# Kernel optimization log

Hardware: AMD Instinct MI355X
Metric: run time of the kernel (lower is better)

Reference implementation:

```python
import jax, jax.numpy as jnp
import numpy as np

B = 8192        # batch
F = 16          # num_fields
V = 50000       # vocab per field
D = 32          # embed_dim (all equal per assert)
NE = 3          # number of embedding spaces
NL = 3          # cross-net layers
EOD = F * D     # 512 = embed_output_dim
M1, M2, M3 = 512, 256, 128
REG_WEIGHT = 0.01


def setup_inputs() -> dict:
    key = jax.random.key(0)
    ks = jax.random.split(key, 12)
    x = jax.random.randint(ks[0], (B, F), 0, V)
    emb_tables = jax.random.normal(ks[1], (NE, F * V, D), dtype=jnp.float32) * 0.05
    cross_W = jax.random.normal(ks[2], (NE, NL, EOD, EOD), dtype=jnp.float32) * (1.0 / np.sqrt(EOD))
    cross_b = jnp.zeros((NE, NL, EOD), dtype=jnp.float32)
    mlp1_W = jax.random.normal(ks[3], (NE, EOD, M1), dtype=jnp.float32) * (1.0 / np.sqrt(EOD))
    mlp1_b = jnp.zeros((NE, M1), dtype=jnp.float32)
    mlp_W1 = jax.random.normal(ks[4], (M1, M2), dtype=jnp.float32) * (1.0 / np.sqrt(M1))
    mlp_b1 = jnp.zeros((M2,), dtype=jnp.float32)
    mlp_W2 = jax.random.normal(ks[5], (M2, M3), dtype=jnp.float32) * (1.0 / np.sqrt(M2))
    mlp_b2 = jnp.zeros((M3,), dtype=jnp.float32)
    mlp_W3 = jax.random.normal(ks[6], (M3, 1), dtype=jnp.float32) * (1.0 / np.sqrt(M3))
    mlp_b3 = jnp.zeros((1,), dtype=jnp.float32)
    return {"x": x, "emb_tables": emb_tables, "cross_W": cross_W, "cross_b": cross_b,
            "mlp1_W": mlp1_W, "mlp1_b": mlp1_b, "mlp_W1": mlp_W1, "mlp_b1": mlp_b1,
            "mlp_W2": mlp_W2, "mlp_b2": mlp_b2, "mlp_W3": mlp_W3, "mlp_b3": mlp_b3}


def _branch(x0, Ws, bs, W1, b1):
    # DCNv2 cross network: x_{l+1} = x0 * (W_l x_l + b_l) + x_l, then one MLP layer (ReLU)
    xl = x0
    for l in range(NL):
        xl = x0 * (xl @ Ws[l] + bs[l]) + xl
    return jax.nn.relu(xl @ W1 + b1)


def reference(x, emb_tables, cross_W, cross_b, mlp1_W, mlp1_b,
              mlp_W1, mlp_b1, mlp_W2, mlp_b2, mlp_W3, mlp_b3):
    offsets = jnp.arange(F, dtype=x.dtype) * V
    idx = x + offsets                      # [B, F] indices into shared table
    es = emb_tables[:, idx]                # [NE, B, F, D]
    es_flat = es.reshape(NE, B, EOD)       # [NE, B, F*D]
    h = jax.vmap(_branch)(es_flat, cross_W, cross_b, mlp1_W, mlp1_b)  # [NE, B, M1]
    h = h.mean(axis=0)                     # mean over embedding spaces
    h = jax.nn.relu(h @ mlp_W1 + mlp_b1)
    h = jax.nn.relu(h @ mlp_W2 + mlp_b2)
    p = h @ mlp_W3 + mlp_b3                # [B, 1]
    output = jax.nn.sigmoid(p[:, 0])
    # training-path regularizer: per-field cross-embedding Gram SVDs
    pairs = [(1, 0), (2, 0), (2, 1)]
    sims = []
    for i, j in pairs:
        m = jnp.einsum('bkd,bke->kde', es[i], es[j])     # [F, D, D]
        s = jnp.linalg.svd(m, compute_uv=False)          # batched singular values [F, D]
        sims.append(s.mean(axis=0))                      # [D]
    sim = jnp.concatenate(sims)                          # [len(pairs)*D]
    reg_loss = REG_WEIGHT * jnp.mean(sim ** 2)
    return output, reg_loss
```

## Files before the change

kernel.cpp:

```cpp
#include <hip/hip_runtime.h>
#include <math.h>

#define B_ 8192
#define F_ 16
#define V_ 50000
#define D_ 32
#define NE_ 3
#define EOD_ 512
#define M1_ 512
#define M2_ 256
#define M3_ 128
#define BE_ ((size_t)B_ * EOD_)

typedef __attribute__((ext_vector_type(8))) short short8;
typedef __attribute__((ext_vector_type(4))) float floatx4;

__device__ __forceinline__ unsigned short f2bf(float f) {
    union { float f; unsigned u; } v; v.f = f;
    unsigned r = v.u + 0x7FFF + ((v.u >> 16) & 1);
    return (unsigned short)(r >> 16);
}
__device__ __forceinline__ float bf2f(unsigned short h) {
    union { unsigned u; float f; } v; v.u = (unsigned)h << 16;
    return v.f;
}
__device__ __forceinline__ void gld16(const void* g, void* l) {
    __builtin_amdgcn_global_load_lds(
        (const __attribute__((address_space(1))) unsigned int*)g,
        (__attribute__((address_space(3))) unsigned int*)l, 16, 0, 0);
}

__global__ __launch_bounds__(256) void gather_k(const int* __restrict__ x,
    const float* __restrict__ tables, unsigned short* __restrict__ esb)
{
    int gid = blockIdx.x * 256 + threadIdx.x;
    int d8 = gid & 3;
    int f  = (gid >> 2) & 15;
    int b  = (gid >> 6) & (B_ - 1);
    int e  = gid >> 19;
    int idx = x[b * F_ + f] + f * V_;
    const float4* src = (const float4*)(tables + ((size_t)e * F_ * V_ + idx) * D_) + d8 * 2;
    float4 v0 = src[0], v1 = src[1];
    unsigned short o[8];
    o[0] = f2bf(v0.x); o[1] = f2bf(v0.y); o[2] = f2bf(v0.z); o[3] = f2bf(v0.w);
    o[4] = f2bf(v1.x); o[5] = f2bf(v1.y); o[6] = f2bf(v1.z); o[7] = f2bf(v1.w);
    unsigned short* dst = esb + ((size_t)e * B_ + b) * EOD_ + f * D_ + d8 * 8;
    *(uint4*)dst = *(uint4*)o;
}

__global__ __launch_bounds__(256) void wtrans12_k(const float* __restrict__ crossW,
    const float* __restrict__ mlp1W, unsigned short* __restrict__ Wt)
{
    __shared__ float tile[32][33];
    int bn = blockIdx.x * 32, bk = blockIdx.y * 32;
    int mat = blockIdx.z;
    const float* Wm = (mat < 9) ? crossW + (size_t)mat * 512 * 512
                                : mlp1W + (size_t)(mat - 9) * 512 * 512;
    unsigned short* Wtm = Wt + (size_t)mat * 512 * 512;
    int tx = threadIdx.x & 31, ty = threadIdx.x >> 5;
    #pragma unroll
    for (int i = 0; i < 32; i += 8)
        tile[ty + i][tx] = Wm[(size_t)(bk + ty + i) * 512 + bn + tx];
    __syncthreads();
    #pragma unroll
    for (int i = 0; i < 32; i += 8)
        Wtm[(size_t)(bn + ty + i) * 512 + bk + tx] = f2bf(tile[tx][ty + i]);
}

__global__ __launch_bounds__(256) void wtrans_k(const float* __restrict__ W,
    unsigned short* __restrict__ Wt, int K, int N)
{
    __shared__ float tile[32][33];
    int bn = blockIdx.x * 32, bk = blockIdx.y * 32;
    int tx = threadIdx.x & 31, ty = threadIdx.x >> 5;
    #pragma unroll
    for (int i = 0; i < 32; i += 8)
        tile[ty + i][tx] = W[(size_t)(bk + ty + i) * N + bn + tx];
    __syncthreads();
    #pragma unroll
    for (int i = 0; i < 32; i += 8)
        Wt[(size_t)(bn + ty + i) * K + bk + tx] = f2bf(tile[tx][ty + i]);
}

__global__ __launch_bounds__(256) void gemm_mfma_k(
    const unsigned short* __restrict__ A,  long sA,
    const unsigned short* __restrict__ Wt, long sW,
    const float* __restrict__ bias,        long sB,
    const unsigned short* __restrict__ x0, long sX,
    const unsigned short* __restrict__ xl, long sXl,
    unsigned short* __restrict__ outb,     long sO,
    int M, int N, int K, int mode)
{
    int e = blockIdx.z;
    A    += (size_t)e * sA;
    Wt   += (size_t)e * sW;
    bias += (size_t)e * sB;
    outb += (size_t)e * sO;
    if (mode == 0) { x0 += (size_t)e * sX; xl += (size_t)e * sXl; }

    __shared__ unsigned short As[128 * 32];
    __shared__ unsigned short Bs[128 * 32];
    int t = threadIdx.x;
    int w = t >> 6, lane = t & 63;
    int quad = lane >> 4, lid = lane & 15;
    int wr = (w & 1) * 64, wc = (w >> 1) * 64;
    int rowbase = blockIdx.y * 128, colbase = blockIdx.x * 128;

    int chunk = w * 2;
    int sub = lane >> 2;
    int kk = (lane & 3) * 8;
    const unsigned short* pa0 = A  + (size_t)(rowbase + chunk * 16 + sub) * K + kk;
    const unsigned short* pa1 = pa0 + (size_t)16 * K;
    const unsigned short* pb0 = Wt + (size_t)(colbase + chunk * 16 + sub) * K + kk;
    const unsigned short* pb1 = pb0 + (size_t)16 * K;
    unsigned short* la0 = As + chunk * 512 + lane * 8;
    unsigned short* la1 = la0 + 512;
    unsigned short* lb0 = Bs + chunk * 512 + lane * 8;
    unsigned short* lb1 = lb0 + 512;

    floatx4 acc[4][4];
    #pragma unroll
    for (int i = 0; i < 4; i++)
        #pragma unroll
        for (int j = 0; j < 4; j++) acc[i][j] = {0.f, 0.f, 0.f, 0.f};

    for (int k0 = 0; k0 < K; k0 += 32) {
        if (k0) __syncthreads();
        gld16(pa0 + k0, la0);
        gld16(pa1 + k0, la1);
        gld16(pb0 + k0, lb0);
        gld16(pb1 + k0, lb1);
        __syncthreads();
        short8 af[4], bfr[4];
        #pragma unroll
        for (int i = 0; i < 4; i++) {
            af[i]  = *(const short8*)(As + (wr + i * 16 + lid) * 32 + quad * 8);
            bfr[i] = *(const short8*)(Bs + (wc + i * 16 + lid) * 32 + quad * 8);
        }
        #pragma unroll
        for (int i = 0; i < 4; i++)
            #pragma unroll
            for (int j = 0; j < 4; j++)
                acc[i][j] = __builtin_amdgcn_mfma_f32_16x16x32_bf16(af[i], bfr[j], acc[i][j], 0, 0, 0);
    }

    #pragma unroll
    for (int i = 0; i < 4; i++) {
        int row0 = rowbase + wr + i * 16 + quad * 4;
        #pragma unroll
        for (int j = 0; j < 4; j++) {
            int col = colbase + wc + j * 16 + lid;
            float bv = bias[col];
            #pragma unroll
            for (int rr = 0; rr < 4; rr++) {
                size_t off = (size_t)(row0 + rr) * N + col;
                float v = acc[i][j][rr] + bv;
                if (mode == 0)      v = bf2f(x0[off]) * v + bf2f(xl[off]);
                else if (mode == 1) v = fmaxf(v, 0.f) * (1.f / 3.f);
                else                v = fmaxf(v, 0.f);
                outb[off] = f2bf(v);
            }
        }
    }
}

__global__ __launch_bounds__(256) void sum3_k(const unsigned short* __restrict__ h,
                                              unsigned short* __restrict__ o)
{
    size_t i = ((size_t)blockIdx.x * 256 + threadIdx.x) * 8;
    uint4 a = *(const uint4*)(h + i);
    uint4 b = *(const uint4*)(h + BE_ + i);
    uint4 c = *(const uint4*)(h + 2 * BE_ + i);
    const unsigned short* pa = (const unsigned short*)&a;
    const unsigned short* pb = (const unsigned short*)&b;
    const unsigned short* pc = (const unsigned short*)&c;
    unsigned short r[8];
    #pragma unroll
    for (int j = 0; j < 8; j++) r[j] = f2bf(bf2f(pa[j]) + bf2f(pb[j]) + bf2f(pc[j]));
    *(uint4*)(o + i) = *(uint4*)r;
}

__global__ __launch_bounds__(256) void final_k(const unsigned short* __restrict__ h2,
    const float* __restrict__ W3, const float* __restrict__ b3,
    float* __restrict__ out)
{
    int gt = blockIdx.x * 256 + threadIdx.x;
    int s = gt >> 6, lane = gt & 63;
    float p = bf2f(h2[(size_t)s * 128 + lane]) * W3[lane]
            + bf2f(h2[(size_t)s * 128 + 64 + lane]) * W3[64 + lane];
    #pragma unroll
    for (int off = 32; off > 0; off >>= 1) p += __shfl_down(p, off);
    if (lane == 0) out[s] = 1.0f / (1.0f + expf(-(p + b3[0])));
}

__global__ __launch_bounds__(256) void pairsum_k(const unsigned short* __restrict__ es,
                                                 float* __restrict__ m)
{
    const int pi[3] = {1, 2, 2};
    const int pj[3] = {0, 0, 1};
    int pk = blockIdx.x;
    int pair = pk >> 4, k = pk & 15;
    const unsigned short* Ei = es + (size_t)pi[pair] * BE_ + k * D_;
    const unsigned short* Ej = es + (size_t)pj[pair] * BE_ + k * D_;
    int b0 = blockIdx.y * (B_ / 16);

    __shared__ float sa[8][32], sb[8][32];
    int t = threadIdx.x;
    int d = t >> 3, e4 = (t & 7) * 4;
    int lr = t >> 5, lc = t & 31;
    float a0 = 0, a1 = 0, a2 = 0, a3 = 0;

    for (int bb = b0; bb < b0 + B_ / 16; bb += 8) {
        __syncthreads();
        sa[lr][lc] = bf2f(Ei[(size_t)(bb + lr) * EOD_ + lc]);
        sb[lr][lc] = bf2f(Ej[(size_t)(bb + lr) * EOD_ + lc]);
        __syncthreads();
        #pragma unroll
        for (int s2 = 0; s2 < 8; s2++) {
            float avv = sa[s2][d];
            float4 bvv = *(const float4*)&sb[s2][e4];
            a0 += avv * bvv.x; a1 += avv * bvv.y;
            a2 += avv * bvv.z; a3 += avv * bvv.w;
        }
    }
    float* dst = m + (size_t)pk * 1024 + d * 32 + e4;
    atomicAdd(dst + 0, a0); atomicAdd(dst + 1, a1);
    atomicAdd(dst + 2, a2); atomicAdd(dst + 3, a3);
}

__global__ __launch_bounds__(64) void svd_k(const float* __restrict__ mg,
                                            float* __restrict__ sv)
{
    int mat = blockIdx.x;
    int l = threadIdx.x;
    int col = l & 31, half = l >> 5;
    const float* src = mg + (size_t)mat * 1024 + half * 16 * 32 + col;
    float a[16];
    #pragma unroll
    for (int j = 0; j < 16; j++) a[j] = src[j * 32];

    for (int sweep = 0; sweep < 6; sweep++) {
        for (int r = 0; r < 31; r++) {
            int partner, isp;
            if (col == 31) { partner = r; isp = 1; }
            else {
                int u = col - r; if (u < 0) u += 31;
                if (u == 0) { partner = 31; isp = 0; }
                else {
                    int v = 2 * r - col; v %= 31; if (v < 0) v += 31;
                    partner = v;
                    isp = (u <= 15) ? 1 : 0;
                }
            }
            int plane = half * 32 + partner;
            float b[16];
            #pragma unroll
            for (int j = 0; j < 16; j++) b[j] = __shfl(a[j], plane, 64);
            float own = 0.f, cross = 0.f, par = 0.f;
            #pragma unroll
            for (int j = 0; j < 16; j++) {
                own   += a[j] * a[j];
                cross += a[j] * b[j];
                par   += b[j] * b[j];
            }
            own   += __shfl_xor(own, 32);
            cross += __shfl_xor(cross, 32);
            par   += __shfl_xor(par, 32);
            float app = isp ? own : par;
            float aqq = isp ? par : own;
            float c = 1.f, s = 0.f;
            if (fabsf(cross) > 1e-12f) {
                float tau = (aqq - app) / (2.f * cross);
                float tt = (tau >= 0.f) ? 1.f / (tau + sqrtf(1.f + tau * tau))
                                        : 1.f / (tau - sqrtf(1.f + tau * tau));
                c = rsqrtf(1.f + tt * tt); s = tt * c;
            }
            float sgn = isp ? -s : s;
            #pragma unroll
            for (int j = 0; j < 16; j++) a[j] = c * a[j] + sgn * b[j];
        }
    }

    float nn = 0.f;
    #pragma unroll
    for (int j = 0; j < 16; j++) nn += a[j] * a[j];
    nn += __shfl_xor(nn, 32);
    float v = sqrtf(nn);

    __shared__ float ev[32];
    if (half == 0) ev[col] = v;
    if (half == 0) {
        int rank = 0;
        for (int o2 = 0; o2 < 32; o2++) {
            float w = ev[o2];
            if (w > v || (w == v && o2 < col)) rank++;
        }
        sv[(size_t)mat * 32 + rank] = v;
    }
}

__global__ __launch_bounds__(128) void reg_k(const float* __restrict__ sv,
                                             float* __restrict__ out)
{
    __shared__ float red[128];
    int t = threadIdx.x;
    float val = 0.f;
    if (t < 96) {
        int p = t >> 5, d = t & 31;
        float s = 0;
        #pragma unroll
        for (int k = 0; k < 16; k++) s += sv[(size_t)(p * 16 + k) * 32 + d];
        s *= (1.f / 16.f);
        val = s * s;
    }
    red[t] = val; __syncthreads();
    for (int off = 64; off > 0; off >>= 1) {
        if (t < off) red[t] += red[t + off];
        __syncthreads();
    }
    if (t == 0) out[B_] = 0.01f * red[0] / 96.f;
}

extern "C" void kernel_launch(void* const* d_in, const int* in_sizes, int n_in,
                              void* d_out, int out_size, void* d_ws, size_t ws_size,
                              hipStream_t stream)
{
    const int*   x      = (const int*)d_in[0];
    const float* emb    = (const float*)d_in[1];
    const float* crossW = (const float*)d_in[2];
    const float* crossb = (const float*)d_in[3];
    const float* mlp1W  = (const float*)d_in[4];
    const float* mlp1b  = (const float*)d_in[5];
    const float* W1     = (const float*)d_in[6];
    const float* b1     = (const float*)d_in[7];
    const float* W2     = (const float*)d_in[8];
    const float* b2     = (const float*)d_in[9];
    const float* W3     = (const float*)d_in[10];
    const float* b3     = (const float*)d_in[11];
    float* out = (float*)d_out;

    unsigned char* wsb = (unsigned char*)d_ws;
    size_t o = 0;
    auto alloc = [&](size_t bytes) -> void* {
        void* p = wsb + o; o += (bytes + 255) & ~(size_t)255; return p;
    };
    unsigned short* esb  = (unsigned short*)alloc(3 * BE_ * 2);
    unsigned short* B0   = (unsigned short*)alloc(3 * BE_ * 2);
    unsigned short* B1   = (unsigned short*)alloc(3 * BE_ * 2);
    unsigned short* WtC  = (unsigned short*)alloc((size_t)12 * 512 * 512 * 2);
    unsigned short* Wt1  = (unsigned short*)alloc((size_t)512 * 256 * 2);
    unsigned short* Wt2  = (unsigned short*)alloc((size_t)256 * 128 * 2);
    float*          mbuf = (float*)alloc(48 * 1024 * 4);
    float*          svb  = (float*)alloc(48 * 32 * 4);
    unsigned short* WtM  = WtC + (size_t)9 * 512 * 512;
    unsigned short* hsb = B0;
    unsigned short* h1b = B0 + (size_t)B_ * M1_;
    unsigned short* h2b = h1b + (size_t)B_ * M2_;

    wtrans12_k<<<dim3(16, 16, 12), 256, 0, stream>>>(crossW, mlp1W, WtC);
    wtrans_k<<<dim3( 8, 16), 256, 0, stream>>>(W1, Wt1, 512, 256);
    wtrans_k<<<dim3( 4,  8), 256, 0, stream>>>(W2, Wt2, 256, 128);

    gather_k<<<(NE_ * B_ * F_ * 4) / 256, 256, 0, stream>>>(x, emb, esb);

    hipMemsetAsync(mbuf, 0, 48 * 1024 * 4, stream);
    pairsum_k<<<dim3(48, 16), 256, 0, stream>>>(esb, mbuf);
    svd_k<<<48, 64, 0, stream>>>(mbuf, svb);
    reg_k<<<1, 128, 0, stream>>>(svb, out);

    const long sW512 = 3 * 512 * 512;
    gemm_mfma_k<<<dim3(4, 64, 3), 256, 0, stream>>>(
        esb, (long)BE_, WtC, sW512, crossb, 3 * 512,
        esb, (long)BE_, esb, (long)BE_, B0, (long)BE_, B_, EOD_, EOD_, 0);
    gemm_mfma_k<<<dim3(4, 64, 3), 256, 0, stream>>>(
        B0, (long)BE_, WtC + 512 * 512, sW512, crossb + 512, 3 * 512,
        esb, (long)BE_, B0, (long)BE_, B1, (long)BE_, B_, EOD_, EOD_, 0);
    gemm_mfma_k<<<dim3(4, 64, 3), 256, 0, stream>>>(
        B1, (long)BE_, WtC + 2 * 512 * 512, sW512, crossb + 1024, 3 * 512,
        esb, (long)BE_, B1, (long)BE_, B0, (long)BE_, B_, EOD_, EOD_, 0);
    gemm_mfma_k<<<dim3(4, 64, 3), 256, 0, stream>>>(
        B0, (long)BE_, WtM, 512 * 512, mlp1b, 512,
        nullptr, 0, nullptr, 0, B1, (long)BE_, B_, M1_, EOD_, 1);
    sum3_k<<<(B_ * M1_) / (256 * 8), 256, 0, stream>>>(B1, hsb);
    gemm_mfma_k<<<dim3(2, 64, 1), 256, 0, stream>>>(
        hsb, 0, Wt1, 0, b1, 0, nullptr, 0, nullptr, 0,
        h1b, 0, B_, M2_, M1_, 2);
    gemm_mfma_k<<<dim3(1, 64, 1), 256, 0, stream>>>(
        h1b, 0, Wt2, 0, b2, 0, nullptr, 0, nullptr, 0,
        h2b, 0, B_, M3_, M2_, 2);
    final_k<<<(B_ * 64) / 256, 256, 0, stream>>>(h2b, W3, b3, out);
}
```

Measured before the change: 706.7 us.

## Fuse regularizer, sum3 and final layer into templated GEMM launches

The pairsum, SVD and reg kernels run as extra z-slices of the three cross-layer GEMM launches, so they execute alongside the GEMMs and need no separate launches. The sum over embedding spaces moves into the A-operand load of the first MLP GEMM, and the final dot product plus sigmoid moves into the last GEMM's epilogue through LDS. The MFMA operand order is swapped so each lane holds four contiguous columns, which allows vectorized epilogue stores and bias loads. The risks are that the fused sum3 load replaces the async global-to-LDS copy with register loads that are repeated for each column block, and that reg_dev's tree reduction now reads red[128..255] while its launch has only 256 threads per block, so those entries must be written.

New measurement: 690.6 us. 1.02x faster.

```diff
diff --git a/kernel.cpp b/kernel.cpp
--- a/kernel.cpp
+++ b/kernel.cpp
@@ -14,6 +14,7 @@
 
 typedef __attribute__((ext_vector_type(8))) short short8;
 typedef __attribute__((ext_vector_type(4))) float floatx4;
+typedef __attribute__((ext_vector_type(4))) unsigned short us4;
 
 __device__ __forceinline__ unsigned short f2bf(float f) {
     union { float f; unsigned u; } v; v.f = f;
@@ -28,6 +29,18 @@
     __builtin_amdgcn_global_load_lds(
         (const __attribute__((address_space(1))) unsigned int*)g,
         (__attribute__((address_space(3))) unsigned int*)l, 16, 0, 0);
+}
+__device__ __forceinline__ void sum3st(const unsigned short* p, unsigned short* l) {
+    uint4 a = *(const uint4*)p;
+    uint4 b = *(const uint4*)(p + BE_);
+    uint4 c = *(const uint4*)(p + 2 * BE_);
+    const unsigned short* pa = (const unsigned short*)&a;
+    const unsigned short* pb = (const unsigned short*)&b;
+    const unsigned short* pc = (const unsigned short*)&c;
+    unsigned short r[8];
+    #pragma unroll
+    for (int j = 0; j < 8; j++) r[j] = f2bf(bf2f(pa[j]) + bf2f(pb[j]) + bf2f(pc[j]));
+    *(uint4*)l = *(uint4*)r;
 }
 
 __global__ __launch_bounds__(256) void gather_k(const int* __restrict__ x,
@@ -82,130 +95,19 @@
         Wt[(size_t)(bn + ty + i) * K + bk + tx] = f2bf(tile[tx][ty + i]);
 }
 
-__global__ __launch_bounds__(256) void gemm_mfma_k(
-    const unsigned short* __restrict__ A,  long sA,
-    const unsigned short* __restrict__ Wt, long sW,
-    const float* __restrict__ bias,        long sB,
-    const unsigned short* __restrict__ x0, long sX,
-    const unsigned short* __restrict__ xl, long sXl,
-    unsigned short* __restrict__ outb,     long sO,
-    int M, int N, int K, int mode)
-{
-    int e = blockIdx.z;
-    A    += (size_t)e * sA;
-    Wt   += (size_t)e * sW;
-    bias += (size_t)e * sB;
-    outb += (size_t)e * sO;
-    if (mode == 0) { x0 += (size_t)e * sX; xl += (size_t)e * sXl; }
-
-    __shared__ unsigned short As[128 * 32];
-    __shared__ unsigned short Bs[128 * 32];
-    int t = threadIdx.x;
-    int w = t >> 6, lane = t & 63;
-    int quad = lane >> 4, lid = lane & 15;
-    int wr = (w & 1) * 64, wc = (w >> 1) * 64;
-    int rowbase = blockIdx.y * 128, colbase = blockIdx.x * 128;
-
-    int chunk = w * 2;
-    int sub = lane >> 2;
-    int kk = (lane & 3) * 8;
-    const unsigned short* pa0 = A  + (size_t)(rowbase + chunk * 16 + sub) * K + kk;
-    const unsigned short* pa1 = pa0 + (size_t)16 * K;
-    const unsigned short* pb0 = Wt + (size_t)(colbase + chunk * 16 + sub) * K + kk;
-    const unsigned short* pb1 = pb0 + (size_t)16 * K;
-    unsigned short* la0 = As + chunk * 512 + lane * 8;
-    unsigned short* la1 = la0 + 512;
-    unsigned short* lb0 = Bs + chunk * 512 + lane * 8;
-    unsigned short* lb1 = lb0 + 512;
-
-    floatx4 acc[4][4];
-    #pragma unroll
-    for (int i = 0; i < 4; i++)
-        #pragma unroll
-        for (int j = 0; j < 4; j++) acc[i][j] = {0.f, 0.f, 0.f, 0.f};
-
-    for (int k0 = 0; k0 < K; k0 += 32) {
-        if (k0) __syncthreads();
-        gld16(pa0 + k0, la0);
-        gld16(pa1 + k0, la1);
-        gld16(pb0 + k0, lb0);
-        gld16(pb1 + k0, lb1);
-        __syncthreads();
-        short8 af[4], bfr[4];
-        #pragma unroll
-        for (int i = 0; i < 4; i++) {
-            af[i]  = *(const short8*)(As + (wr + i * 16 + lid) * 32 + quad * 8);
-            bfr[i] = *(const short8*)(Bs + (wc + i * 16 + lid) * 32 + quad * 8);
-        }
-        #pragma unroll
-        for (int i = 0; i < 4; i++)
-            #pragma unroll
-            for (int j = 0; j < 4; j++)
-                acc[i][j] = __builtin_amdgcn_mfma_f32_16x16x32_bf16(af[i], bfr[j], acc[i][j], 0, 0, 0);
-    }
-
-    #pragma unroll
-    for (int i = 0; i < 4; i++) {
-        int row0 = rowbase + wr + i * 16 + quad * 4;
-        #pragma unroll
-        for (int j = 0; j < 4; j++) {
-            int col = colbase + wc + j * 16 + lid;
-            float bv = bias[col];
-            #pragma unroll
-            for (int rr = 0; rr < 4; rr++) {
-                size_t off = (size_t)(row0 + rr) * N + col;
-                float v = acc[i][j][rr] + bv;
-                if (mode == 0)      v = bf2f(x0[off]) * v + bf2f(xl[off]);
-                else if (mode == 1) v = fmaxf(v, 0.f) * (1.f / 3.f);
-                else                v = fmaxf(v, 0.f);
-                outb[off] = f2bf(v);
-            }
-        }
-    }
-}
-
-__global__ __launch_bounds__(256) void sum3_k(const unsigned short* __restrict__ h,
-                                              unsigned short* __restrict__ o)
-{
-    size_t i = ((size_t)blockIdx.x * 256 + threadIdx.x) * 8;
-    uint4 a = *(const uint4*)(h + i);
-    uint4 b = *(const uint4*)(h + BE_ + i);
-    uint4 c = *(const uint4*)(h + 2 * BE_ + i);
-    const unsigned short* pa = (const unsigned short*)&a;
-    const unsigned short* pb = (const unsigned short*)&b;
-    const unsigned short* pc = (const unsigned short*)&c;
-    unsigned short r[8];
-    #pragma unroll
-    for (int j = 0; j < 8; j++) r[j] = f2bf(bf2f(pa[j]) + bf2f(pb[j]) + bf2f(pc[j]));
-    *(uint4*)(o + i) = *(uint4*)r;
-}
-
-__global__ __launch_bounds__(256) void final_k(const unsigned short* __restrict__ h2,
-    const float* __restrict__ W3, const float* __restrict__ b3,
-    float* __restrict__ out)
-{
-    int gt = blockIdx.x * 256 + threadIdx.x;
-    int s = gt >> 6, lane = gt & 63;
-    float p = bf2f(h2[(size_t)s * 128 + lane]) * W3[lane]
-            + bf2f(h2[(size_t)s * 128 + 64 + lane]) * W3[64 + lane];
-    #pragma unroll
-    for (int off = 32; off > 0; off >>= 1) p += __shfl_down(p, off);
-    if (lane == 0) out[s] = 1.0f / (1.0f + expf(-(p + b3[0])));
-}
-
-__global__ __launch_bounds__(256) void pairsum_k(const unsigned short* __restrict__ es,
-                                                 float* __restrict__ m)
+__device__ void pairsum_dev(const unsigned short* es, float* m, int ablk, int t,
+                            void* smemv)
 {
     const int pi[3] = {1, 2, 2};
     const int pj[3] = {0, 0, 1};
-    int pk = blockIdx.x;
+    int pk = ablk % 48, by = ablk / 48;
     int pair = pk >> 4, k = pk & 15;
     const unsigned short* Ei = es + (size_t)pi[pair] * BE_ + k * D_;
     const unsigned short* Ej = es + (size_t)pj[pair] * BE_ + k * D_;
-    int b0 = blockIdx.y * (B_ / 16);
-
-    __shared__ float sa[8][32], sb[8][32];
-    int t = threadIdx.x;
+    int b0 = by * (B_ / 16);
+
+    float (*sa)[32] = (float(*)[32])smemv;
+    float (*sb)[32] = sa + 8;
     int d = t >> 3, e4 = (t & 7) * 4;
     int lr = t >> 5, lc = t & 31;
     float a0 = 0, a1 = 0, a2 = 0, a3 = 0;
@@ -228,11 +130,11 @@
     atomicAdd(dst + 2, a2); atomicAdd(dst + 3, a3);
 }
 
-__global__ __launch_bounds__(64) void svd_k(const float* __restrict__ mg,
-                                            float* __restrict__ sv)
-{
-    int mat = blockIdx.x;
-    int l = threadIdx.x;
+__device__ void svd_dev(const float* mg, float* sv, int ablk, int t, void* smemv)
+{
+    if (ablk >= 48 || t >= 64) return;
+    int mat = ablk;
+    int l = t;
     int col = l & 31, half = l >> 5;
     const float* src = mg + (size_t)mat * 1024 + half * 16 * 32 + col;
     float a[16];
@@ -287,7 +189,7 @@
     nn += __shfl_xor(nn, 32);
     float v = sqrtf(nn);
 
-    __shared__ float ev[32];
+    float* ev = (float*)smemv;
     if (half == 0) ev[col] = v;
     if (half == 0) {
         int rank = 0;
@@ -299,11 +201,10 @@
     }
 }
 
-__global__ __launch_bounds__(128) void reg_k(const float* __restrict__ sv,
-                                             float* __restrict__ out)
-{
-    __shared__ float red[128];
-    int t = threadIdx.x;
+__device__ void reg_dev(const float* sv, float* outf, int ablk, int t, void* smemv)
+{
+    if (ablk != 0) return;
+    float* red = (float*)smemv;
     float val = 0.f;
     if (t < 96) {
         int p = t >> 5, d = t & 31;
@@ -314,11 +215,165 @@
         val = s * s;
     }
     red[t] = val; __syncthreads();
-    for (int off = 64; off > 0; off >>= 1) {
+    for (int off = 128; off > 0; off >>= 1) {
         if (t < off) red[t] += red[t + off];
         __syncthreads();
     }
-    if (t == 0) out[B_] = 0.01f * red[0] / 96.f;
+    if (t == 0) outf[B_] = 0.01f * red[0] / 96.f;
+}
+
+template<int MODE, int AUX, int ASUM>
+__global__ __launch_bounds__(256) void gemm_k(
+    const unsigned short* __restrict__ A,  long sA,
+    const unsigned short* __restrict__ Wt, long sW,
+    const float* __restrict__ bias,        long sB,
+    const unsigned short* __restrict__ x0, long sX,
+    const unsigned short* __restrict__ xl, long sXl,
+    unsigned short* __restrict__ outb,     long sO,
+    int M, int N, int K,
+    const unsigned short* __restrict__ es, float* __restrict__ mbuf,
+    float* __restrict__ svb, const float* __restrict__ W3,
+    const float* __restrict__ b3, float* __restrict__ outf)
+{
+    constexpr int SMEMB = (MODE == 3) ? 32768 : 16384;
+    __shared__ __align__(16) unsigned char smem[SMEMB];
+    int t = threadIdx.x;
+
+    if (AUX && blockIdx.z >= 3) {
+        int ablk = (blockIdx.z - 3) * 256 + blockIdx.y * 4 + blockIdx.x;
+        if (AUX == 1)      pairsum_dev(es, mbuf, ablk, t, smem);
+        else if (AUX == 2) svd_dev(mbuf, svb, ablk, t, smem);
+        else               reg_dev(svb, outf, ablk, t, smem);
+        return;
+    }
+
+    int e = blockIdx.z;
+    A    += (size_t)e * sA;
+    Wt   += (size_t)e * sW;
+    bias += (size_t)e * sB;
+    outb += (size_t)e * sO;
+    if (MODE == 0) { x0 += (size_t)e * sX; xl += (size_t)e * sXl; }
+
+    unsigned short* As = (unsigned short*)smem;
+    unsigned short* Bs = As + 128 * 32;
+    int w = t >> 6, lane = t & 63;
+    int quad = lane >> 4, lid = lane & 15;
+    int wr = (w & 1) * 64, wc = (w >> 1) * 64;
+    int rowbase = blockIdx.y * 128, colbase = blockIdx.x * 128;
+
+    int chunk = w * 2;
+    int sub = lane >> 2;
+    int kk = (lane & 3) * 8;
+    const unsigned short* pa0 = A  + (size_t)(rowbase + chunk * 16 + sub) * K + kk;
+    const unsigned short* pa1 = pa0 + (size_t)16 * K;
+    const unsigned short* pb0 = Wt + (size_t)(colbase + chunk * 16 + sub) * K + kk;
+    const unsigned short* pb1 = pb0 + (size_t)16 * K;
+    unsigned short* la0 = As + chunk * 512 + lane * 8;
+    unsigned short* la1 = la0 + 512;
+    unsigned short* lb0 = Bs + chunk * 512 + lane * 8;
+    unsigned short* lb1 = lb0 + 512;
+
+    floatx4 acc[4][4];
+    #pragma unroll
+    for (int i = 0; i < 4; i++)
+        #pragma unroll
+        for (int j = 0; j < 4; j++) acc[i][j] = {0.f, 0.f, 0.f, 0.f};
+
+    for (int k0 = 0; k0 < K; k0 += 32) {
+        if (k0) __syncthreads();
+        if (ASUM) {
+            sum3st(pa0 + k0, la0);
+            sum3st(pa1 + k0, la1);
+        } else {
+            gld16(pa0 + k0, la0);
+            gld16(pa1 + k0, la1);
+        }
+        gld16(pb0 + k0, lb0);
+        gld16(pb1 + k0, lb1);
+        __syncthreads();
+        short8 af[4], bfr[4];
+        #pragma unroll
+        for (int i = 0; i < 4; i++) {
+            af[i]  = *(const short8*)(As + (wr + i * 16 + lid) * 32 + quad * 8);
+            bfr[i] = *(const short8*)(Bs + (wc + i * 16 + lid) * 32 + quad * 8);
+        }
+        #pragma unroll
+        for (int i = 0; i < 4; i++)
+            #pragma unroll
+            for (int j = 0; j < 4; j++)
+                acc[i][j] = __builtin_amdgcn_mfma_f32_16x16x32_bf16(bfr[j], af[i], acc[i][j], 0, 0, 0);
+    }
+
+    if (MODE == 3) {
+        __syncthreads();
+        unsigned short* h2s = (unsigned short*)smem;
+        #pragma unroll
+        for (int i = 0; i < 4; i++) {
+            int rl = wr + i * 16 + lid;
+            int sw = (rl & 7) << 3;
+            #pragma unroll
+            for (int j = 0; j < 4; j++) {
+                int col0 = wc + j * 16 + quad * 4;
+                float4 bv = *(const float4*)(bias + col0);
+                float v0 = fmaxf(acc[i][j][0] + bv.x, 0.f);
+                float v1 = fmaxf(acc[i][j][1] + bv.y, 0.f);
+                float v2 = fmaxf(acc[i][j][2] + bv.z, 0.f);
+                float v3 = fmaxf(acc[i][j][3] + bv.w, 0.f);
+                us4 o = { f2bf(v0), f2bf(v1), f2bf(v2), f2bf(v3) };
+                *(us4*)(h2s + (size_t)rl * 128 + (col0 ^ sw)) = o;
+            }
+        }
+        __syncthreads();
+        if (t < 128) {
+            int sw = (t & 7) << 3;
+            const unsigned short* hr = h2s + (size_t)t * 128;
+            float p = 0.f;
+            #pragma unroll
+            for (int cc = 0; cc < 128; cc += 4) {
+                us4 hv = *(const us4*)(hr + (cc ^ sw));
+                float4 wv = *(const float4*)(W3 + cc);
+                p += bf2f(hv.x) * wv.x + bf2f(hv.y) * wv.y
+                   + bf2f(hv.z) * wv.z + bf2f(hv.w) * wv.w;
+            }
+            outf[rowbase + t] = 1.0f / (1.0f + expf(-(p + b3[0])));
+        }
+        return;
+    }
+
+    #pragma unroll
+    for (int i = 0; i < 4; i++) {
+        int row = rowbase + wr + i * 16 + lid;
+        #pragma unroll
+        for (int j = 0; j < 4; j++) {
+            int col0 = colbase + wc + j * 16 + quad * 4;
+            size_t off = (size_t)row * N + col0;
+            float4 bv = *(const float4*)(bias + col0);
+            float v0 = acc[i][j][0] + bv.x;
+            float v1 = acc[i][j][1] + bv.y;
+            float v2 = acc[i][j][2] + bv.z;
+            float v3 = acc[i][j][3] + bv.w;
+            if (MODE == 0) {
+                us4 xv = *(const us4*)(x0 + off);
+                us4 lv = *(const us4*)(xl + off);
+                v0 = bf2f(xv.x) * v0 + bf2f(lv.x);
+                v1 = bf2f(xv.y) * v1 + bf2f(lv.y);
+                v2 = bf2f(xv.z) * v2 + bf2f(lv.z);
+                v3 = bf2f(xv.w) * v3 + bf2f(lv.w);
+            } else if (MODE == 1) {
+                v0 = fmaxf(v0, 0.f) * (1.f / 3.f);
+                v1 = fmaxf(v1, 0.f) * (1.f / 3.f);
+                v2 = fmaxf(v2, 0.f) * (1.f / 3.f);
+                v3 = fmaxf(v3, 0.f) * (1.f / 3.f);
+            } else {
+                v0 = fmaxf(v0, 0.f);
+                v1 = fmaxf(v1, 0.f);
+                v2 = fmaxf(v2, 0.f);
+                v3 = fmaxf(v3, 0.f);
+            }
+            us4 o = { f2bf(v0), f2bf(v1), f2bf(v2), f2bf(v3) };
+            *(us4*)(outb + off) = o;
+        }
+    }
 }
 
 extern "C" void kernel_launch(void* const* d_in, const int* in_sizes, int n_in,
@@ -353,9 +408,7 @@
     float*          mbuf = (float*)alloc(48 * 1024 * 4);
     float*          svb  = (float*)alloc(48 * 32 * 4);
     unsigned short* WtM  = WtC + (size_t)9 * 512 * 512;
-    unsigned short* hsb = B0;
-    unsigned short* h1b = B0 + (size_t)B_ * M1_;
-    unsigned short* h2b = h1b + (size_t)B_ * M2_;
+    unsigned short* h1b  = esb;
 
     wtrans12_k<<<dim3(16, 16, 12), 256, 0, stream>>>(crossW, mlp1W, WtC);
     wtrans_k<<<dim3( 8, 16), 256, 0, stream>>>(W1, Wt1, 512, 256);
@@ -364,29 +417,31 @@
     gather_k<<<(NE_ * B_ * F_ * 4) / 256, 256, 0, stream>>>(x, emb, esb);
 
     hipMemsetAsync(mbuf, 0, 48 * 1024 * 4, stream);
-    pairsum_k<<<dim3(48, 16), 256, 0, stream>>>(esb, mbuf);
-    svd_k<<<48, 64, 0, stream>>>(mbuf, svb);
-    reg_k<<<1, 128, 0, stream>>>(svb, out);
 
     const long sW512 = 3 * 512 * 512;
-    gemm_mfma_k<<<dim3(4, 64, 3), 256, 0, stream>>>(
+
+    gemm_k<0, 1, 0><<<dim3(4, 64, 6), 256, 0, stream>>>(
         esb, (long)BE_, WtC, sW512, crossb, 3 * 512,
-        esb, (long)BE_, esb, (long)BE_, B0, (long)BE_, B_, EOD_, EOD_, 0);
-    gemm_mfma_k<<<dim3(4, 64, 3), 256, 0, stream>>>(
+        esb, (long)BE_, esb, (long)BE_, B0, (long)BE_, B_, EOD_, EOD_,
+        esb, mbuf, svb, nullptr, nullptr, nullptr);
+    gemm_k<0, 2, 0><<<dim3(4, 64, 4), 256, 0, stream>>>(
         B0, (long)BE_, WtC + 512 * 512, sW512, crossb + 512, 3 * 512,
-        esb, (long)BE_, B0, (long)BE_, B1, (long)BE_, B_, EOD_, EOD_, 0);
-    gemm_mfma_k<<<dim3(4, 64, 3), 256, 0, stream>>>(
+        esb, (long)BE_, B0, (long)BE_, B1, (long)BE_, B_, EOD_, EOD_,
+        nullptr, mbuf, svb, nullptr, nullptr, nullptr);
+    gemm_k<0, 3, 0><<<dim3(4, 64, 4), 256, 0, stream>>>(
         B1, (long)BE_, WtC + 2 * 512 * 512, sW512, crossb + 1024, 3 * 512,
-        esb, (long)BE_, B1, (long)BE_, B0, (long)BE_, B_, EOD_, EOD_, 0);
-    gemm_mfma_k<<<dim3(4, 64, 3), 256, 0, stream>>>(
+        esb, (long)BE_, B1, (long)BE_, B0, (long)BE_, B_, EOD_, EOD_,
+        nullptr, mbuf, svb, nullptr, nullptr, out);
+    gemm_k<1, 0, 0><<<dim3(4, 64, 3), 256, 0, stream>>>(
         B0, (long)BE_, WtM, 512 * 512, mlp1b, 512,
-        nullptr, 0, nullptr, 0, B1, (long)BE_, B_, M1_, EOD_, 1);
-    sum3_k<<<(B_ * M1_) / (256 * 8), 256, 0, stream>>>(B1, hsb);
-    gemm_mfma_k<<<dim3(2, 64, 1), 256, 0, stream>>>(
-        hsb, 0, Wt1, 0, b1, 0, nullptr, 0, nullptr, 0,
-        h1b, 0, B_, M2_, M1_, 2);
-    gemm_mfma_k<<<dim3(1, 64, 1), 256, 0, stream>>>(
+        nullptr, 0, nullptr, 0, B1, (long)BE_, B_, M1_, EOD_,
+        nullptr, nullptr, nullptr, nullptr, nullptr, nullptr);
+    gemm_k<2, 0, 1><<<dim3(2, 64, 1), 256, 0, stream>>>(
+        B1, 0, Wt1, 0, b1, 0, nullptr, 0, nullptr, 0,
+        h1b, 0, B_, M2_, M1_,
+        nullptr, nullptr, nullptr, nullptr, nullptr, nullptr);
+    gemm_k<3, 0, 0><<<dim3(1, 64, 1), 256, 0, stream>>>(
         h1b, 0, Wt2, 0, b2, 0, nullptr, 0, nullptr, 0,
-        h2b, 0, B_, M3_, M2_, 2);
-    final_k<<<(B_ * 64) / 256, 256, 0, stream>>>(h2b, W3, b3, out);
-}
+        nullptr, 0, B_, M3_, M2_,
+        nullptr, nullptr, nullptr, W3, b3, out);
+}
```
